# Kernel optimization log

Hardware: AMD Instinct MI355X
Metric: run time of the kernel (lower is better)

## Reference

```python
import jax, jax.numpy as jnp
import numpy as np

B, L, D, H = 2, 2048, 1024, 16
HD = D // H  # head_dim = 64


def setup_inputs() -> dict:
    key = jax.random.key(0)
    ks = jax.random.split(key, 6)
    return {
        "q": jax.random.normal(ks[0], (B, L, D), dtype=jnp.float32),
        "k": jax.random.normal(ks[1], (B, L, D), dtype=jnp.float32),
        "v": jax.random.normal(ks[2], (B, L, D), dtype=jnp.float32),
        "Wq": jax.random.normal(ks[3], (D, D), dtype=jnp.float32) * (D ** -0.5),
        "Wk": jax.random.normal(ks[4], (D, D), dtype=jnp.float32) * (D ** -0.5),
        "Wv": jax.random.normal(ks[5], (D, D), dtype=jnp.float32) * (D ** -0.5),
    }


def reference(q, k, v, Wq, Wk, Wv):
    # nn.Linear(bias=False): y = x @ W.T ; then split heads -> [B,H,L,HD]
    def proj(x, W):
        return (x @ W.T).reshape(B, L, H, HD).transpose(0, 2, 1, 3)

    Q = proj(q, Wq)
    K = proj(k, Wk)
    V = proj(v, Wv)
    scale = HD ** -0.5
    idx = jnp.arange(L)
    # flex_attention score_mod: score + (q_idx - kv_idx), applied after scaling
    bias = (idx[:, None] - idx[None, :]).astype(q.dtype)  # [L, L]
    scores = jnp.einsum('bhqd,bhkd->bhqk', Q, K) * scale + bias
    attn = jax.nn.softmax(scores, axis=-1)
    out = jnp.einsum('bhqk,bhkd->bhqd', attn, V)
    # 'b h l d -> b l (h d)'
    return out.transpose(0, 2, 1, 3).reshape(B, L, D)
```

## Files before the change

kernel.cpp:

```cpp
#include <hip/hip_runtime.h>

#define DEVFN __device__ __forceinline__

typedef __attribute__((ext_vector_type(8))) short bf16x8;
typedef __attribute__((ext_vector_type(4))) float f32x4;

constexpr int cB = 2, cL = 2048, cD = 1024, cH = 16, cHD = 64;
constexpr int ELE   = 4194304;
constexpr int WELE  = 1048576;
constexpr int KWIN  = 128;
constexpr int SLICE = 2 * KWIN * cD;

#if __has_builtin(__builtin_amdgcn_exp2f)
#define EXP2F(x) __builtin_amdgcn_exp2f(x)
#else
#define EXP2F(x) __expf(0.6931471805599453f * (x))
#endif

DEVFN unsigned short hu(float f) {
  return (unsigned short)((__float_as_uint(f) + 0x8000u) >> 16);
}
DEVFN unsigned pkhu(float a, float b) {
  unsigned ua = __float_as_uint(a) + 0x8000u;
  unsigned ub = __float_as_uint(b) + 0x8000u;
  return __builtin_amdgcn_perm(ub, ua, 0x07060302u);
}

#if __has_builtin(__builtin_amdgcn_global_load_lds)
#define HAVE_ASYNC 1
typedef const __attribute__((address_space(1))) unsigned int* gas1_t;
typedef __attribute__((address_space(3))) unsigned int* las3_t;
#define ASYNC_CP16(g, l) \
  __builtin_amdgcn_global_load_lds((gas1_t)(g), (las3_t)(l), 16, 0, 0)
#else
#define HAVE_ASYNC 0
#endif

DEVFN int swzofs(int row, int cc) { return row * 64 + (((cc) ^ (row & 7)) << 3); }

__global__ __launch_bounds__(256)
void conv_bf16(const float* __restrict__ q, const float* __restrict__ k,
               const float* __restrict__ v, const float* __restrict__ Wq,
               const float* __restrict__ Wk, const float* __restrict__ Wv,
               unsigned short* __restrict__ qb, unsigned short* __restrict__ kb,
               unsigned short* __restrict__ vb, unsigned short* __restrict__ wb) {
  const int y = blockIdx.y;
  const int i8 = (blockIdx.x * 256 + threadIdx.x) * 8;
  const float* src; unsigned short* dst; int n;
  size_t sofs = i8, dofs = i8;
  switch (y) {
    case 0:  src = q;  dst = qb;          n = ELE;  break;
    case 1:  case 2: {
      n = SLICE;
      const size_t b = (size_t)(i8 >> 17);
      sofs = b * ((size_t)cL * cD) + (i8 & (KWIN * cD - 1));
      src = (y == 1) ? k : v;  dst = (y == 1) ? kb : vb;  break;
    }
    case 3:  src = Wq; dst = wb;          n = WELE; break;
    case 4:  src = Wk; dst = wb + WELE;   n = WELE; break;
    default: src = Wv; dst = wb + 2*WELE; n = WELE; break;
  }
  if (i8 >= n) return;
  float4 a = *(const float4*)(src + sofs);
  float4 b4 = *(const float4*)(src + sofs + 4);
  uint4 o = {pkhu(a.x, a.y), pkhu(a.z, a.w), pkhu(b4.x, b4.y), pkhu(b4.z, b4.w)};
  *(uint4*)(dst + dofs) = o;
}

__global__ __launch_bounds__(256)
void proj_kv(const unsigned short* __restrict__ xk,
             const unsigned short* __restrict__ xv,
             const unsigned short* __restrict__ wAll,
             unsigned short* __restrict__ Kc,
             unsigned short* __restrict__ Vc) {
  __shared__ __align__(16) unsigned short As[128 * 64];
  __shared__ __align__(16) unsigned short Bs[64 * 64];
  const int tid = threadIdx.x;
  const int wv = tid >> 6, lane = tid & 63, id = lane & 15, quad = lane >> 4;
  const int wr = wv >> 1, wc = wv & 1;
  const int rl = lane >> 3, cc = (lane & 7) ^ rl;

  const int bx = blockIdx.x;
  int mode, M0, N0;
  const unsigned short *A, *B;
  unsigned short* outp;
  if (bx < 32) {
    mode = 1; A = xk; B = wAll + WELE; outp = Kc;
    M0 = (bx & 1) * KWIN;
    N0 = (bx >> 1) * 64;
  } else {
    const int t = bx - 32;
    mode = 2; A = wAll + 2 * WELE; B = xv; outp = Vc;
    M0 = (t & 7) * 128;
    const int y = t >> 3;
    N0 = (y >> 1) * KWIN + (y & 1) * 64;
  }

  f32x4 acc[4][2];
#pragma unroll
  for (int i = 0; i < 4; ++i)
#pragma unroll
    for (int j = 0; j < 2; ++j) acc[i][j] = (f32x4){0.f, 0.f, 0.f, 0.f};

  for (int k0 = 0; k0 < cD; k0 += 64) {
#if HAVE_ASYNC
    __syncthreads();
#pragma unroll
    for (int c = 0; c < 4; ++c)
      ASYNC_CP16(A + (size_t)(M0 + c * 32 + wv * 8 + rl) * cD + k0 + cc * 8,
                 &As[(c * 32 + wv * 8) * 64]);
#pragma unroll
    for (int c = 0; c < 2; ++c)
      ASYNC_CP16(B + (size_t)(N0 + c * 32 + wv * 8 + rl) * cD + k0 + cc * 8,
                 &Bs[(c * 32 + wv * 8) * 64]);
    __syncthreads();
#else
    uint4 ra[4], rb[2];
#pragma unroll
    for (int c = 0; c < 4; ++c)
      ra[c] = *(const uint4*)(A + (size_t)(M0 + c * 32 + wv * 8 + rl) * cD + k0 + cc * 8);
#pragma unroll
    for (int c = 0; c < 2; ++c)
      rb[c] = *(const uint4*)(B + (size_t)(N0 + c * 32 + wv * 8 + rl) * cD + k0 + cc * 8);
    __syncthreads();
#pragma unroll
    for (int c = 0; c < 4; ++c) *(uint4*)&As[(c * 32 + wv * 8) * 64 + lane * 8] = ra[c];
#pragma unroll
    for (int c = 0; c < 2; ++c) *(uint4*)&Bs[(c * 32 + wv * 8) * 64 + lane * 8] = rb[c];
    __syncthreads();
#endif

#pragma unroll
    for (int ks = 0; ks < 2; ++ks) {
      bf16x8 af[4], bfr[2];
#pragma unroll
      for (int mi = 0; mi < 4; ++mi)
        af[mi] = *(const bf16x8*)&As[swzofs(wr * 64 + mi * 16 + id, ks * 4 + quad)];
#pragma unroll
      for (int ni = 0; ni < 2; ++ni)
        bfr[ni] = *(const bf16x8*)&Bs[swzofs(wc * 32 + ni * 16 + id, ks * 4 + quad)];
#pragma unroll
      for (int mi = 0; mi < 4; ++mi)
#pragma unroll
        for (int ni = 0; ni < 2; ++ni)
          acc[mi][ni] = __builtin_amdgcn_mfma_f32_16x16x32_bf16(
              af[mi], bfr[ni], acc[mi][ni], 0, 0, 0);
    }
  }

#pragma unroll
  for (int mi = 0; mi < 4; ++mi) {
#pragma unroll
    for (int ni = 0; ni < 2; ++ni) {
#pragma unroll
      for (int rg = 0; rg < 4; ++rg) {
        const int mr = M0 + wr * 64 + mi * 16 + quad * 4 + rg;
        const int nc = N0 + wc * 32 + ni * 16 + id;
        size_t idx;
        if (mode == 1) {
          const int b = mr >> 7, l = mr & 127, h = nc >> 6, hd = nc & 63;
          idx = ((size_t)((b * cH + h) * KWIN + l)) * cHD + hd;
        } else {
          const int h = mr >> 6, hd = mr & 63, b = nc >> 7, l = nc & 127;
          idx = ((size_t)((b * cH + h) * cHD + hd)) * KWIN + l;
        }
        outp[idx] = hu(acc[mi][ni][rg]);
      }
    }
  }
}

__global__ __launch_bounds__(512)
void fused_qattn(const unsigned short* __restrict__ Xq,
                 const unsigned short* __restrict__ Wq,
                 const unsigned short* __restrict__ Kc,
                 const unsigned short* __restrict__ Vc,
                 float* __restrict__ out) {
  __shared__ __align__(16) unsigned short lds[36864];
  unsigned short* As = lds;
  unsigned short* Bs = lds + 8192;
  unsigned short* Ks = lds + 12288;
  unsigned short* Vs = lds + 20480;
  unsigned short* Ps = lds + 28672;

  const int tid = threadIdx.x;
  const int wv = tid >> 6, lane = tid & 63, id = lane & 15, quad = lane >> 4;
  const int wr = wv >> 1, wc = wv & 1;
  const int rl = lane >> 3, cc = (lane & 7) ^ rl;
  const int bh = blockIdx.y, q0 = blockIdx.x * 128;
  const int bb = bh >> 4, h = bh & 15;
  const size_t M0 = (size_t)bb * cL + q0;
  const unsigned short* Bw = Wq + (size_t)(h * cHD) * cD;
  const unsigned short* Kb = Kc + (size_t)bh * KWIN * cHD;
  const unsigned short* Vb = Vc + (size_t)bh * cHD * KWIN;

  const int rbase = wv * 8;

#if HAVE_ASYNC
#pragma unroll
  for (int c = 0; c < 2; ++c)
    ASYNC_CP16(Kb + (size_t)(c * 64 + rbase + rl) * cHD + cc * 8,
               &Ks[(c * 64 + rbase) * 64]);
#pragma unroll
  for (int it = 0; it < 2; ++it)
    ASYNC_CP16(Vb + (size_t)(rbase + rl) * KWIN + it * 64 + cc * 8,
               &Vs[it * 4096 + rbase * 64]);
#else
  {
    uint4 kv0r = *(const uint4*)(Kb + (size_t)(rbase + rl) * cHD + cc * 8);
    uint4 kv1r = *(const uint4*)(Kb + (size_t)(64 + rbase + rl) * cHD + cc * 8);
    uint4 vv0r = *(const uint4*)(Vb + (size_t)(rbase + rl) * KWIN + cc * 8);
    uint4 vv1r = *(const uint4*)(Vb + (size_t)(rbase + rl) * KWIN + 64 + cc * 8);
    *(uint4*)&Ks[rbase * 64 + lane * 8] = kv0r;
    *(uint4*)&Ks[(64 + rbase) * 64 + lane * 8] = kv1r;
    *(uint4*)&Vs[rbase * 64 + lane * 8] = vv0r;
    *(uint4*)&Vs[4096 + rbase * 64 + lane * 8] = vv1r;
  }
#endif

  f32x4 acc[2][2];
#pragma unroll
  for (int i = 0; i < 2; ++i)
#pragma unroll
    for (int j = 0; j < 2; ++j) acc[i][j] = (f32x4){0.f, 0.f, 0.f, 0.f};

  for (int k0 = 0; k0 < cD; k0 += 64) {
#if HAVE_ASYNC
    __syncthreads();
#pragma unroll
    for (int c = 0; c < 2; ++c)
      ASYNC_CP16(Xq + (M0 + c * 64 + wv * 8 + rl) * cD + k0 + cc * 8,
                 &As[(c * 64 + wv * 8) * 64]);
    ASYNC_CP16(Bw + (size_t)(wv * 8 + rl) * cD + k0 + cc * 8,
               &Bs[(wv * 8) * 64]);
    __syncthreads();
#else
    uint4 ra[2], rb1;
#pragma unroll
    for (int c = 0; c < 2; ++c)
      ra[c] = *(const uint4*)(Xq + (M0 + c * 64 + wv * 8 + rl) * cD + k0 + cc * 8);
    rb1 = *(const uint4*)(Bw + (size_t)(wv * 8 + rl) * cD + k0 + cc * 8);
    __syncthreads();
#pragma unroll
    for (int c = 0; c < 2; ++c) *(uint4*)&As[(c * 64 + wv * 8) * 64 + lane * 8] = ra[c];
    *(uint4*)&Bs[(wv * 8) * 64 + lane * 8] = rb1;
    __syncthreads();
#endif

#pragma unroll
    for (int ks = 0; ks < 2; ++ks) {
      bf16x8 af[2], bfr[2];
#pragma unroll
      for (int mi = 0; mi < 2; ++mi)
        af[mi] = *(const bf16x8*)&As[swzofs(wr * 32 + mi * 16 + id, ks * 4 + quad)];
#pragma unroll
      for (int ni = 0; ni < 2; ++ni)
        bfr[ni] = *(const bf16x8*)&Bs[swzofs(wc * 32 + ni * 16 + id, ks * 4 + quad)];
#pragma unroll
      for (int mi = 0; mi < 2; ++mi)
#pragma unroll
        for (int ni = 0; ni < 2; ++ni)
          acc[mi][ni] = __builtin_amdgcn_mfma_f32_16x16x32_bf16(
              af[mi], bfr[ni], acc[mi][ni], 0, 0, 0);
    }
  }

  __syncthreads();
#pragma unroll
  for (int mi = 0; mi < 2; ++mi)
#pragma unroll
    for (int ni = 0; ni < 2; ++ni)
#pragma unroll
      for (int rg = 0; rg < 4; ++rg) {
        const int qrow = wr * 32 + mi * 16 + quad * 4 + rg;
        const int col  = wc * 32 + ni * 16 + id;
        As[swzofs(qrow, col >> 3) + (col & 7)] = hu(acc[mi][ni][rg]);
      }
  __syncthreads();

  bf16x8 aq[2];
#pragma unroll
  for (int ks = 0; ks < 2; ++ks)
    aq[ks] = *(const bf16x8*)&As[swzofs(wv * 16 + id, ks * 4 + quad)];

  constexpr float L2E = 1.4426950408889634f;
  constexpr float SC2 = 0.125f * L2E;

  f32x4 oacc[4];
#pragma unroll
  for (int i = 0; i < 4; ++i) oacc[i] = (f32x4){0.f, 0.f, 0.f, 0.f};
  float m_i[4], l_i[4];
#pragma unroll
  for (int i = 0; i < 4; ++i) { m_i[i] = -1e30f; l_i[i] = 0.f; }

  for (int it = 0; it < 2; ++it) {
    const int kv0 = it * 64;

    f32x4 sa[4];
#pragma unroll
    for (int nt = 0; nt < 4; ++nt) sa[nt] = (f32x4){0.f, 0.f, 0.f, 0.f};
#pragma unroll
    for (int ks = 0; ks < 2; ++ks)
#pragma unroll
      for (int nt = 0; nt < 4; ++nt) {
        bf16x8 kf = *(const bf16x8*)&Ks[swzofs(kv0 + nt * 16 + id, ks * 4 + quad)];
        sa[nt] = __builtin_amdgcn_mfma_f32_16x16x32_bf16(aq[ks], kf, sa[nt], 0, 0, 0);
      }

    const float tkv = (float)(kv0 + id) * L2E;
    float negkb[4];
#pragma unroll
    for (int nt = 0; nt < 4; ++nt) negkb[nt] = -(tkv + (float)(nt * 16) * L2E);

    float z[4][4], mt[4];
#pragma unroll
    for (int i = 0; i < 4; ++i) {
#pragma unroll
      for (int nt = 0; nt < 4; ++nt)
        z[i][nt] = fmaf(sa[nt][i], SC2, negkb[nt]);
      mt[i] = fmaxf(fmaxf(z[i][0], z[i][1]), fmaxf(z[i][2], z[i][3]));
    }
#pragma unroll
    for (int mk = 1; mk < 16; mk <<= 1)
#pragma unroll
      for (int i = 0; i < 4; ++i)
        mt[i] = fmaxf(mt[i], __shfl_xor(mt[i], mk));

    float p[4][4], rs[4], al[4];
#pragma unroll
    for (int i = 0; i < 4; ++i) {
      const float mn = fmaxf(m_i[i], mt[i]);
      al[i] = EXP2F(m_i[i] - mn);
      m_i[i] = mn;
      float s = 0.f;
#pragma unroll
      for (int nt = 0; nt < 4; ++nt) { p[i][nt] = EXP2F(z[i][nt] - mn); s += p[i][nt]; }
      rs[i] = s;
    }
#pragma unroll
    for (int mk = 1; mk < 16; mk <<= 1)
#pragma unroll
      for (int i = 0; i < 4; ++i) rs[i] += __shfl_xor(rs[i], mk);
#pragma unroll
    for (int i = 0; i < 4; ++i) l_i[i] = l_i[i] * al[i] + rs[i];
#pragma unroll
    for (int nh = 0; nh < 4; ++nh)
#pragma unroll
      for (int i = 0; i < 4; ++i) oacc[nh][i] *= al[i];

#pragma unroll
    for (int i = 0; i < 4; ++i) {
      const int qrow = wv * 16 + quad * 4 + i;
#pragma unroll
      for (int nt = 0; nt < 4; ++nt) {
        const int col = nt * 16 + id;
        Ps[swzofs(qrow, col >> 3) + (col & 7)] = hu(p[i][nt]);
      }
    }

    bf16x8 pf[2];
#pragma unroll
    for (int ks2 = 0; ks2 < 2; ++ks2)
      pf[ks2] = *(const bf16x8*)&Ps[swzofs(wv * 16 + id, ks2 * 4 + quad)];
#pragma unroll
    for (int ks2 = 0; ks2 < 2; ++ks2)
#pragma unroll
      for (int nh = 0; nh < 4; ++nh) {
        bf16x8 vf = *(const bf16x8*)&Vs[it * 4096 + swzofs(nh * 16 + id, ks2 * 4 + quad)];
        oacc[nh] = __builtin_amdgcn_mfma_f32_16x16x32_bf16(pf[ks2], vf, oacc[nh], 0, 0, 0);
      }
  }

#pragma unroll
  for (int i = 0; i < 4; ++i) {
    const float inv = 1.0f / l_i[i];
    const int qrow = q0 + wv * 16 + quad * 4 + i;
    float* op = out + ((size_t)(bb * cL + qrow)) * cD + h * cHD + id;
#pragma unroll
    for (int nh = 0; nh < 4; ++nh)
      op[nh * 16] = oacc[nh][i] * inv;
  }
}

extern "C" void kernel_launch(void* const* d_in, const int* in_sizes, int n_in,
                              void* d_out, int out_size, void* d_ws, size_t ws_size,
                              hipStream_t stream) {
  const float* q  = (const float*)d_in[0];
  const float* k  = (const float*)d_in[1];
  const float* v  = (const float*)d_in[2];
  const float* Wq = (const float*)d_in[3];
  const float* Wk = (const float*)d_in[4];
  const float* Wv = (const float*)d_in[5];
  float* out = (float*)d_out;

  unsigned short* Qb  = (unsigned short*)d_ws;
  unsigned short* Wb  = Qb + ELE;
  unsigned short* Ksl = Wb + 3 * WELE;
  unsigned short* Vsl = Ksl + SLICE;
  unsigned short* Kc  = Vsl + SLICE;
  unsigned short* Vc  = Kc + SLICE;

  conv_bf16<<<dim3(2048, 6), dim3(256), 0, stream>>>(q, k, v, Wq, Wk, Wv,
                                                     Qb, Ksl, Vsl, Wb);
  proj_kv<<<dim3(64), dim3(256), 0, stream>>>(Ksl, Vsl, Wb, Kc, Vc);
  fused_qattn<<<dim3(16, 32), dim3(512), 0, stream>>>(Qb, Wb, Kc, Vc, out);
}
```

Measured before the change: 135.1 us.

## Double-buffer the Q-projection GEMM tiles in LDS

Adds a second LDS buffer for the X and Wq tiles, so the next k-tile is staged while MFMAs run on the current one. The loop is fully unrolled and uses one barrier per iteration instead of two. LDS grows from 72KB to 80KB and the region layout is rearranged, with Ps now aliasing the B buffers, which may reduce occupancy. In the non-async path the global loads are not held in registers across the compute, so overlap there relies on the compiler scheduling them.

Result: no change. 133.1 us (-1.5%).

```diff
diff --git a/kernel.cpp b/kernel.cpp
--- a/kernel.cpp
+++ b/kernel.cpp
@@ -176,12 +176,10 @@
                  const unsigned short* __restrict__ Kc,
                  const unsigned short* __restrict__ Vc,
                  float* __restrict__ out) {
-  __shared__ __align__(16) unsigned short lds[36864];
-  unsigned short* As = lds;
-  unsigned short* Bs = lds + 8192;
-  unsigned short* Ks = lds + 12288;
-  unsigned short* Vs = lds + 20480;
-  unsigned short* Ps = lds + 28672;
+  __shared__ __align__(16) unsigned short lds[40960];
+  unsigned short* Ks = lds + 24576;
+  unsigned short* Vs = lds + 32768;
+  unsigned short* Ps = lds + 16384;
 
   const int tid = threadIdx.x;
   const int wv = tid >> 6, lane = tid & 63, id = lane & 15, quad = lane >> 4;
@@ -218,44 +216,57 @@
   }
 #endif
 
+#if HAVE_ASYNC
+#define STAGE_TILE(buf, k0)                                                    \
+  {                                                                            \
+    unsigned short* A_ = lds + (buf) * 8192;                                   \
+    unsigned short* B_ = lds + 16384 + (buf) * 4096;                           \
+    _Pragma("unroll")                                                          \
+    for (int c = 0; c < 2; ++c)                                                \
+      ASYNC_CP16(Xq + (M0 + c * 64 + wv * 8 + rl) * cD + (k0) + cc * 8,        \
+                 &A_[(c * 64 + wv * 8) * 64]);                                 \
+    ASYNC_CP16(Bw + (size_t)(wv * 8 + rl) * cD + (k0) + cc * 8,                \
+               &B_[(wv * 8) * 64]);                                            \
+  }
+#else
+#define STAGE_TILE(buf, k0)                                                    \
+  {                                                                            \
+    unsigned short* A_ = lds + (buf) * 8192;                                   \
+    unsigned short* B_ = lds + 16384 + (buf) * 4096;                           \
+    uint4 ra0 = *(const uint4*)(Xq + (M0 + 0 * 64 + wv * 8 + rl) * cD + (k0) + cc * 8); \
+    uint4 ra1 = *(const uint4*)(Xq + (M0 + 1 * 64 + wv * 8 + rl) * cD + (k0) + cc * 8); \
+    uint4 rb1 = *(const uint4*)(Bw + (size_t)(wv * 8 + rl) * cD + (k0) + cc * 8);       \
+    *(uint4*)&A_[(0 * 64 + wv * 8) * 64 + lane * 8] = ra0;                     \
+    *(uint4*)&A_[(1 * 64 + wv * 8) * 64 + lane * 8] = ra1;                     \
+    *(uint4*)&B_[(wv * 8) * 64 + lane * 8] = rb1;                              \
+  }
+#endif
+
   f32x4 acc[2][2];
 #pragma unroll
   for (int i = 0; i < 2; ++i)
 #pragma unroll
     for (int j = 0; j < 2; ++j) acc[i][j] = (f32x4){0.f, 0.f, 0.f, 0.f};
 
-  for (int k0 = 0; k0 < cD; k0 += 64) {
-#if HAVE_ASYNC
-    __syncthreads();
-#pragma unroll
-    for (int c = 0; c < 2; ++c)
-      ASYNC_CP16(Xq + (M0 + c * 64 + wv * 8 + rl) * cD + k0 + cc * 8,
-                 &As[(c * 64 + wv * 8) * 64]);
-    ASYNC_CP16(Bw + (size_t)(wv * 8 + rl) * cD + k0 + cc * 8,
-               &Bs[(wv * 8) * 64]);
-    __syncthreads();
-#else
-    uint4 ra[2], rb1;
-#pragma unroll
-    for (int c = 0; c < 2; ++c)
-      ra[c] = *(const uint4*)(Xq + (M0 + c * 64 + wv * 8 + rl) * cD + k0 + cc * 8);
-    rb1 = *(const uint4*)(Bw + (size_t)(wv * 8 + rl) * cD + k0 + cc * 8);
-    __syncthreads();
-#pragma unroll
-    for (int c = 0; c < 2; ++c) *(uint4*)&As[(c * 64 + wv * 8) * 64 + lane * 8] = ra[c];
-    *(uint4*)&Bs[(wv * 8) * 64 + lane * 8] = rb1;
-    __syncthreads();
-#endif
-
+  STAGE_TILE(0, 0);
+  __syncthreads();
+
+#pragma unroll
+  for (int t = 0; t < 16; ++t) {
+    const int cur = t & 1;
+    if (t < 15) STAGE_TILE(cur ^ 1, (t + 1) * 64);
+
+    const unsigned short* A_ = lds + cur * 8192;
+    const unsigned short* B_ = lds + 16384 + cur * 4096;
 #pragma unroll
     for (int ks = 0; ks < 2; ++ks) {
       bf16x8 af[2], bfr[2];
 #pragma unroll
       for (int mi = 0; mi < 2; ++mi)
-        af[mi] = *(const bf16x8*)&As[swzofs(wr * 32 + mi * 16 + id, ks * 4 + quad)];
+        af[mi] = *(const bf16x8*)&A_[swzofs(wr * 32 + mi * 16 + id, ks * 4 + quad)];
 #pragma unroll
       for (int ni = 0; ni < 2; ++ni)
-        bfr[ni] = *(const bf16x8*)&Bs[swzofs(wc * 32 + ni * 16 + id, ks * 4 + quad)];
+        bfr[ni] = *(const bf16x8*)&B_[swzofs(wc * 32 + ni * 16 + id, ks * 4 + quad)];
 #pragma unroll
       for (int mi = 0; mi < 2; ++mi)
 #pragma unroll
@@ -263,9 +274,9 @@
           acc[mi][ni] = __builtin_amdgcn_mfma_f32_16x16x32_bf16(
               af[mi], bfr[ni], acc[mi][ni], 0, 0, 0);
     }
-  }
-
-  __syncthreads();
+    __syncthreads();
+  }
+
 #pragma unroll
   for (int mi = 0; mi < 2; ++mi)
 #pragma unroll
@@ -274,14 +285,14 @@
       for (int rg = 0; rg < 4; ++rg) {
         const int qrow = wr * 32 + mi * 16 + quad * 4 + rg;
         const int col  = wc * 32 + ni * 16 + id;
-        As[swzofs(qrow, col >> 3) + (col & 7)] = hu(acc[mi][ni][rg]);
+        lds[swzofs(qrow, col >> 3) + (col & 7)] = hu(acc[mi][ni][rg]);
       }
   __syncthreads();
 
   bf16x8 aq[2];
 #pragma unroll
   for (int ks = 0; ks < 2; ++ks)
-    aq[ks] = *(const bf16x8*)&As[swzofs(wv * 16 + id, ks * 4 + quad)];
+    aq[ks] = *(const bf16x8*)&lds[swzofs(wv * 16 + id, ks * 4 + quad)];
 
   constexpr float L2E = 1.4426950408889634f;
   constexpr float SC2 = 0.125f * L2E;
```
